# Kernel optimization log

Measured on AMD Instinct MI355X. Metric: run time of the kernel, lower is better.

Reference implementation:

```python
import jax, jax.numpy as jnp
import numpy as np

W, M, N, K = 8, 4096, 4096, 1792  # world_size, tokens, d_model, per-rank K shard


def setup_inputs() -> dict:
    key = jax.random.key(0)
    k1, k2 = jax.random.split(key)
    # Per-rank activations and per-rank weight shards (row-parallel linear).
    inp = jax.random.normal(k1, (W, M, K), dtype=jnp.float32) * 0.05
    wgt = jax.random.normal(k2, (W, N, K), dtype=jnp.float32) * 0.05
    return {"input": inp, "weight": wgt}


def reference(input, weight):
    # Per rank r: partial_r = input_r @ weight_r.T  -> [M, N]
    # All-reduce (sum over ranks) fused into the contraction.
    return jnp.einsum("rmk,rnk->mn", input, weight)
```

## Files before the change

### kernel.cpp

```cpp
#include <hip/hip_runtime.h>
#include <hip/hip_bf16.h>


#define Wsz 8
#define Mdim 4096
#define Ndim 4096
#define Kshard 1792
#define KTOT 14336
#define LDSBUF 32768
#define MK ((size_t)Mdim * Kshard)

typedef __attribute__((ext_vector_type(8))) short short8;
typedef __attribute__((ext_vector_type(4))) float f32x4;

struct Stage { float4 a0l, a0h, a1l, a1h, b0l, b0h, b1l, b1h; };

__global__ void __launch_bounds__(512, 2) gemm_fused(const float* __restrict__ A,
                                                     const float* __restrict__ B,
                                                     float* __restrict__ C) {
    extern __shared__ char smem[];

    const int tid = threadIdx.x;
    const int w = tid >> 6, lane = tid & 63;
    const int l15 = lane & 15, quad = lane >> 4;
    const int wm = (w >> 1) * 64;
    const int wn = (w & 1) * 128;

    const int wgid = (blockIdx.x & 7) * 32 + (blockIdx.x >> 3);
    const long bm = (long)(wgid >> 4) * 256, bn = (long)(wgid & 15) * 256;

    const int g = w * 64 + lane;
    const int sr = g >> 2;
    const int sq = (g & 3) ^ ((sr >> 1) & 3);
    const float* aRow0 = A + (size_t)(bm + sr) * Kshard + sq * 8;
    const float* aRow1 = aRow0 + (size_t)128 * Kshard;
    const float* bRow0 = B + (size_t)(bn + sr) * Kshard + sq * 8;
    const float* bRow1 = bRow0 + (size_t)128 * Kshard;
    const int ldsWr = g * 16;

    const int swz = (quad ^ ((l15 >> 1) & 3)) * 16;
    const int aoff = (wm + l15) * 64 + swz;
    const int boff = 16384 + (wn + l15) * 64 + swz;

    f32x4 acc[4][8] = {};

#define ISSUE(S, off)                                           \
    do {                                                        \
        S.a0l = *(const float4*)(aRow0 + (off));                \
        S.a0h = *(const float4*)(aRow0 + (off) + 4);            \
        S.a1l = *(const float4*)(aRow1 + (off));                \
        S.a1h = *(const float4*)(aRow1 + (off) + 4);            \
        S.b0l = *(const float4*)(bRow0 + (off));                \
        S.b0h = *(const float4*)(bRow0 + (off) + 4);            \
        S.b1l = *(const float4*)(bRow1 + (off));                \
        S.b1h = *(const float4*)(bRow1 + (off) + 4);            \
    } while (0)

#define CV4(dst, lo, hi)                                                          \
    do {                                                                          \
        asm("v_cvt_pk_bf16_f32 %0, %1, %2" : "=v"(dst.x) : "v"(lo.x), "v"(lo.y)); \
        asm("v_cvt_pk_bf16_f32 %0, %1, %2" : "=v"(dst.y) : "v"(lo.z), "v"(lo.w)); \
        asm("v_cvt_pk_bf16_f32 %0, %1, %2" : "=v"(dst.z) : "v"(hi.x), "v"(hi.y)); \
        asm("v_cvt_pk_bf16_f32 %0, %1, %2" : "=v"(dst.w) : "v"(hi.z), "v"(hi.w)); \
    } while (0)

#define CONVWRITE(S, base)                                      \
    do {                                                        \
        uint4 oA0, oA1, oB0, oB1;                               \
        CV4(oA0, S.a0l, S.a0h);                                 \
        CV4(oA1, S.a1l, S.a1h);                                 \
        CV4(oB0, S.b0l, S.b0h);                                 \
        CV4(oB1, S.b1l, S.b1h);                                 \
        *(uint4*)(smem + (base) + ldsWr) = oA0;                 \
        *(uint4*)(smem + (base) + 8192 + ldsWr) = oA1;          \
        *(uint4*)(smem + (base) + 16384 + ldsWr) = oB0;         \
        *(uint4*)(smem + (base) + 24576 + ldsWr) = oB1;         \
    } while (0)

#define COMPUTE(bufbase)                                                                 \
    do {                                                                                 \
        short8 af[4], bfr[8];                                                            \
        _Pragma("unroll") for (int i = 0; i < 4; ++i)                                    \
            af[i] = *(const short8*)(smem + (bufbase) + aoff + i * 1024);                \
        _Pragma("unroll") for (int i = 0; i < 8; ++i)                                    \
            bfr[i] = *(const short8*)(smem + (bufbase) + boff + i * 1024);               \
        _Pragma("unroll") for (int mi = 0; mi < 4; ++mi)                                 \
            _Pragma("unroll") for (int ni = 0; ni < 8; ++ni)                             \
                acc[mi][ni] = __builtin_amdgcn_mfma_f32_16x16x32_bf16(af[mi], bfr[ni],   \
                                                                      acc[mi][ni], 0, 0, 0); \
    } while (0)

#define ADV() do { kkI += 32; if (kkI == Kshard) { kkI = 0; baseI += MK; } } while (0)
#define SB() __builtin_amdgcn_sched_barrier(0)
#define WAIT_VM8() asm volatile("s_waitcnt vmcnt(8)" ::: "memory")
#define WAIT_VM0() asm volatile("s_waitcnt vmcnt(0)" ::: "memory")
#define ENDSTEP()  asm volatile("s_waitcnt lgkmcnt(0)\ns_barrier" ::: "memory")

    Stage S0, S1;
    size_t baseI = 0;
    int kkI = 32;

    ISSUE(S0, 0);
    ISSUE(S1, 32);
    WAIT_VM8(); SB();
    CONVWRITE(S0, 0);
    ENDSTEP(); SB();

    for (int blk = 0; blk < 222; ++blk) {
        ADV(); ISSUE(S0, baseI + kkI); SB();
        COMPUTE(0);
        WAIT_VM8(); SB();
        CONVWRITE(S1, LDSBUF);
        ENDSTEP(); SB();
        ADV(); ISSUE(S1, baseI + kkI); SB();
        COMPUTE(LDSBUF);
        WAIT_VM8(); SB();
        CONVWRITE(S0, 0);
        ENDSTEP(); SB();
    }

    ADV(); ISSUE(S0, baseI + kkI); SB();
    COMPUTE(0);
    WAIT_VM8(); SB();
    CONVWRITE(S1, LDSBUF);
    ENDSTEP(); SB();

    ADV(); ISSUE(S1, baseI + kkI); SB();
    COMPUTE(LDSBUF);
    WAIT_VM8(); SB();
    CONVWRITE(S0, 0);
    ENDSTEP(); SB();

    COMPUTE(0);
    WAIT_VM0(); SB();
    CONVWRITE(S1, LDSBUF);
    ENDSTEP(); SB();

    COMPUTE(LDSBUF);

#undef ISSUE
#undef CV4
#undef CONVWRITE
#undef COMPUTE
#undef ADV
#undef SB
#undef WAIT_VM8
#undef WAIT_VM0
#undef ENDSTEP

#pragma unroll
    for (int mi = 0; mi < 4; ++mi)
#pragma unroll
        for (int ni = 0; ni < 8; ++ni) {
            const long col = bn + wn + ni * 16 + l15;
#pragma unroll
            for (int r2 = 0; r2 < 4; ++r2) {
                const long row = bm + wm + mi * 16 + quad * 4 + r2;
                C[row * Ndim + col] = acc[mi][ni][r2];
            }
        }
}

extern "C" void kernel_launch(void* const* d_in, const int* in_sizes, int n_in,
                              void* d_out, int out_size, void* d_ws, size_t ws_size,
                              hipStream_t stream) {
    const float* inp = (const float*)d_in[0];
    const float* wgt = (const float*)d_in[1];
    float* out = (float*)d_out;

    hipFuncSetAttribute(reinterpret_cast<const void*>(gemm_fused),
                        hipFuncAttributeMaxDynamicSharedMemorySize, 2 * LDSBUF);
    gemm_fused<<<256, 512, 2 * LDSBUF, stream>>>(inp, wgt, out);
}
```

Baseline: 912.9 us.

## Deepen LDS pipeline to four buffers and drop sched barriers

Moves from a double-buffered LDS pipeline to a four-stage ring. Each step writes the tile two stages ahead, issues the next global loads and then computes on the current buffer, so there is only one barrier per step. It also removes the sched_barrier fences so the compiler can interleave loads, conversions and MFMAs. The cost is four times 32KB of LDS per block; with launch bounds of 2 blocks per CU this may reduce occupancy to one block per CU.

Result: slower. 2.704 ms (+196.2%).

```diff
diff --git a/kernel.cpp b/kernel.cpp
--- a/kernel.cpp
+++ b/kernel.cpp
@@ -91,59 +91,52 @@
     } while (0)
 
 #define ADV() do { kkI += 32; if (kkI == Kshard) { kkI = 0; baseI += MK; } } while (0)
-#define SB() __builtin_amdgcn_sched_barrier(0)
 #define WAIT_VM8() asm volatile("s_waitcnt vmcnt(8)" ::: "memory")
 #define WAIT_VM0() asm volatile("s_waitcnt vmcnt(0)" ::: "memory")
 #define ENDSTEP()  asm volatile("s_waitcnt lgkmcnt(0)\ns_barrier" ::: "memory")
 
     Stage S0, S1;
     size_t baseI = 0;
-    int kkI = 32;
+    int kkI = 96;
 
     ISSUE(S0, 0);
     ISSUE(S1, 32);
-    WAIT_VM8(); SB();
+    WAIT_VM8();
     CONVWRITE(S0, 0);
-    ENDSTEP(); SB();
+    ISSUE(S0, 64);
+    WAIT_VM8();
+    CONVWRITE(S1, LDSBUF);
+    ISSUE(S1, 96);
+    ENDSTEP();
 
-    for (int blk = 0; blk < 222; ++blk) {
-        ADV(); ISSUE(S0, baseI + kkI); SB();
-        COMPUTE(0);
-        WAIT_VM8(); SB();
-        CONVWRITE(S1, LDSBUF);
-        ENDSTEP(); SB();
-        ADV(); ISSUE(S1, baseI + kkI); SB();
-        COMPUTE(LDSBUF);
-        WAIT_VM8(); SB();
-        CONVWRITE(S0, 0);
-        ENDSTEP(); SB();
+#define STEP(u, Sx)                                   \
+    do {                                              \
+        WAIT_VM8();                 \
+        CONVWRITE(Sx, (((u) + 2) & 3) * LDSBUF);      \
+        ADV();                                        \
+        ISSUE(Sx, baseI + kkI);           \
+        COMPUTE((u) * LDSBUF);                        \
+        ENDSTEP();                                    \
+    } while (0)
+
+    for (int blk = 0; blk < 111; ++blk) {
+        STEP(0, S0);
+        STEP(1, S1);
+        STEP(2, S0);
+        STEP(3, S1);
     }
+#undef STEP
 
-    ADV(); ISSUE(S0, baseI + kkI); SB();
-    COMPUTE(0);
-    WAIT_VM8(); SB();
-    CONVWRITE(S1, LDSBUF);
-    ENDSTEP(); SB();
-
-    ADV(); ISSUE(S1, baseI + kkI); SB();
-    COMPUTE(LDSBUF);
-    WAIT_VM8(); SB();
-    CONVWRITE(S0, 0);
-    ENDSTEP(); SB();
-
-    COMPUTE(0);
-    WAIT_VM0(); SB();
-    CONVWRITE(S1, LDSBUF);
-    ENDSTEP(); SB();
-
-    COMPUTE(LDSBUF);
+    WAIT_VM8(); CONVWRITE(S0, 2 * LDSBUF); COMPUTE(0);          ENDSTEP();
+    WAIT_VM0(); CONVWRITE(S1, 3 * LDSBUF); COMPUTE(LDSBUF);     ENDSTEP();
+    COMPUTE(2 * LDSBUF); ENDSTEP();
+    COMPUTE(3 * LDSBUF);
 
 #undef ISSUE
 #undef CV4
 #undef CONVWRITE
 #undef COMPUTE
 #undef ADV
-#undef SB
 #undef WAIT_VM8
 #undef WAIT_VM0
 #undef ENDSTEP
@@ -169,6 +162,6 @@
     float* out = (float*)d_out;
 
     hipFuncSetAttribute(reinterpret_cast<const void*>(gemm_fused),
-                        hipFuncAttributeMaxDynamicSharedMemorySize, 2 * LDSBUF);
-    gemm_fused<<<256, 512, 2 * LDSBUF, stream>>>(inp, wgt, out);
+                        hipFuncAttributeMaxDynamicSharedMemorySize, 4 * LDSBUF);
+    gemm_fused<<<256, 512, 4 * LDSBUF, stream>>>(inp, wgt, out);
 }
```
